# Kernel optimization log

Hardware: AMD Instinct MI355X
Metric: run time of the kernel (lower is better)

The kernel has to match this reference:

```python
import jax, jax.numpy as jnp
import numpy as np

N = 50000      # nodes
E = 1600000    # edges (before self loops)
F = 128        # input_dim
H = 4          # num_heads
D = 32         # hidden_dim (per head)
B = 16         # graphs in batch
NEG_SLOPE = 0.2  # PyG GATv2Conv default negative_slope


def setup_inputs() -> dict:
    key = jax.random.key(0)
    ks = jax.random.split(key, 8)
    x = jax.random.normal(ks[0], (N, F), dtype=jnp.float32)
    edge_index = jax.random.randint(ks[1], (2, E), 0, N, dtype=jnp.int32)
    batch = jnp.sort(jax.random.randint(ks[2], (N,), 0, B, dtype=jnp.int32))
    s = 0.05
    W_l = jax.random.normal(ks[3], (F, H * D), dtype=jnp.float32) * s
    b_l = jnp.zeros((H * D,), dtype=jnp.float32)
    W_r = jax.random.normal(ks[4], (F, H * D), dtype=jnp.float32) * s
    b_r = jnp.zeros((H * D,), dtype=jnp.float32)
    att = jax.random.normal(ks[5], (H, D), dtype=jnp.float32) * s
    bias = jnp.zeros((H * D,), dtype=jnp.float32)
    return {"x": x, "edge_index": edge_index, "batch": batch,
            "W_l": W_l, "b_l": b_l, "W_r": W_r, "b_r": b_r,
            "att": att, "bias": bias}


def reference(x, edge_index, batch, W_l, b_l, W_r, b_r, att, bias):
    n = x.shape[0]
    # PyG GATv2Conv adds self loops by default
    loops = jnp.arange(n, dtype=edge_index.dtype)
    src = jnp.concatenate([edge_index[0], loops])  # message source j
    dst = jnp.concatenate([edge_index[1], loops])  # message target i

    xl = (x @ W_l + b_l).reshape(n, H, D)  # source transform
    xr = (x @ W_r + b_r).reshape(n, H, D)  # target transform

    # per-edge GATv2 attention logits: a^T LeakyReLU(xl_j + xr_i)
    m = xl[src] + xr[dst]                                   # [E+N, H, D]
    e = jnp.sum(jax.nn.leaky_relu(m, NEG_SLOPE) * att, -1)  # [E+N, H]

    # softmax over incoming edges of each destination node
    e_max = jax.ops.segment_max(e, dst, num_segments=n)
    ex = jnp.exp(e - e_max[dst])
    den = jax.ops.segment_sum(ex, dst, num_segments=n)
    alpha = ex / den[dst]                                   # [E+N, H]

    # weighted scatter-sum aggregation of source features
    out = jax.ops.segment_sum(alpha[..., None] * xl[src], dst, num_segments=n)
    out = out.reshape(n, H * D) + bias                      # concat heads + bias
    out = jax.nn.relu(out)

    # global max pool over nodes of each graph
    pooled = jax.ops.segment_max(out, batch, num_segments=B)
    pooled = jnp.where(jnp.isfinite(pooled), pooled, 0.0)   # guard empty graphs
    return pooled
```

## Files before the change

kernel.cpp:

```cpp
#include <hip/hip_runtime.h>

#define NN 50000
#define NE 1600000
#define FDIM 128
#define CDIM 128
#define NGRAPH 16
#define SLOPE 0.2f
#define CSTRIDE 96
#define BINSH 7
#define NBIN 391
#define EPB 6400
#define NB1 250
#define EPT 25
#define CAP 5120
#define POOL_NODES 64
#define POOL_NB ((NN + POOL_NODES - 1) / POOL_NODES)
#define TNB 782
#define LOG2E 1.4426950408889634f


__device__ __forceinline__ unsigned short f2bf(float f) {
    unsigned u = __float_as_uint(f);
    return (unsigned short)((u + 0x7FFFu + ((u >> 16) & 1u)) >> 16);
}
__device__ __forceinline__ unsigned packbf(float a, float b) {
    return (unsigned)f2bf(a) | ((unsigned)f2bf(b) << 16);
}
__device__ __forceinline__ unsigned short f2h(float f) {
    union { _Float16 h; unsigned short u; } c;
    c.h = (_Float16)f;
    return c.u;
}

typedef __attribute__((ext_vector_type(8))) short short8;
typedef __attribute__((ext_vector_type(4))) float f32x4;
typedef _Float16 h2 __attribute__((ext_vector_type(2)));
union FragU { uint4 u; short8 s; };
union HU    { uint4 u; h2 h[4]; };
union HI    { h2 h; int i; };

__device__ __forceinline__ float qadd_xor1(float d) {
#if __has_builtin(__builtin_amdgcn_update_dpp)
    int x = __builtin_amdgcn_update_dpp(0, __float_as_int(d), 0xB1, 0xF, 0xF, true);
    return d + __int_as_float(x);
#else
    return d + __shfl_xor(d, 1);
#endif
}
__device__ __forceinline__ float qadd_xor2(float d) {
#if __has_builtin(__builtin_amdgcn_update_dpp)
    int x = __builtin_amdgcn_update_dpp(0, __float_as_int(d), 0x4E, 0xF, 0xF, true);
    return d + __int_as_float(x);
#else
    return d + __shfl_xor(d, 2);
#endif
}
__device__ __forceinline__ float exp2fast(float d) {
#if __has_builtin(__builtin_amdgcn_exp2f)
    return __builtin_amdgcn_exp2f(d);
#else
    return __expf(d * 0.6931471805599453f);
#endif
}

__global__ __launch_bounds__(256) void k_init(
    float* __restrict__ out, int* __restrict__ gbin_cnt,
    const float* __restrict__ Wl, const float* __restrict__ Wr,
    uint4* __restrict__ wpack) {
    const int b = blockIdx.x;
    if (b < 16) {
        int C = b * 256 + threadIdx.x;
        const float* W = (C < 2048) ? Wl : Wr;
        int c = C & 2047;
        int ccol = c & 15, cq = (c >> 4) & 3, ckq = (c >> 6) & 3, cnt_ = c >> 8;
        const float* wp = &W[(size_t)(ckq * 32 + cq * 8) * CDIM + cnt_ * 16 + ccol];
        uint4 u;
        u.x = packbf(wp[0],        wp[CDIM]);
        u.y = packbf(wp[2*CDIM],   wp[3*CDIM]);
        u.z = packbf(wp[4*CDIM],   wp[5*CDIM]);
        u.w = packbf(wp[6*CDIM],   wp[7*CDIM]);
        wpack[C] = u;
    } else {
        int i = (b - 16) * 256 + threadIdx.x;
        if (i < NGRAPH * CDIM) out[i] = 0.f;
        if (i < NBIN) gbin_cnt[i] = 0;
    }
}

__global__ __launch_bounds__(256) void k_front(
    const float* __restrict__ x,
    const float* __restrict__ bl, const float* __restrict__ br,
    const int* __restrict__ src, const int* __restrict__ dst,
    int* __restrict__ gbin_cnt, unsigned* __restrict__ gstage,
    unsigned short* __restrict__ xlh, unsigned short* __restrict__ xrh,
    const uint4* __restrict__ wpack) {
    __shared__ __align__(16) char shraw[32768];
    const int tid = threadIdx.x;

    if (blockIdx.x < NB1) {
        int* bcnt = (int*)shraw;
        int* boff = bcnt + NBIN;
        int* gb   = boff + NBIN;
        int* sc   = gb + NBIN;
        unsigned* st = (unsigned*)(sc + 256);
        const int t  = tid;
        const int e0 = blockIdx.x * EPB;

        for (int b = t; b < NBIN; b += 256) bcnt[b] = 0;
        __syncthreads();

        unsigned sd[EPT]; int bn[EPT]; int pl[EPT];
#pragma unroll
        for (int k = 0; k < EPT; k++) {
            int e = e0 + k * 256 + t;
            int s = src[e], d = dst[e];
            bn[k] = d >> BINSH;
            sd[k] = (unsigned)s | ((unsigned)(d & 127) << 16)
                                | ((unsigned)bn[k] << 23);
            pl[k] = atomicAdd(&bcnt[bn[k]], 1);
        }
        __syncthreads();

        int c0 = (2*t     < NBIN) ? bcnt[2*t]     : 0;
        int c1 = (2*t + 1 < NBIN) ? bcnt[2*t + 1] : 0;
        int v  = c0 + c1;
        sc[t] = v; __syncthreads();
        for (int off = 1; off < 256; off <<= 1) {
            int add = (t >= off) ? sc[t - off] : 0;
            __syncthreads();
            sc[t] += add;
            __syncthreads();
        }
        int base = sc[t] - v;
        if (2*t     < NBIN) boff[2*t]     = base;
        if (2*t + 1 < NBIN) boff[2*t + 1] = base + c0;
        __syncthreads();

        for (int b = t; b < NBIN; b += 256) {
            int c = bcnt[b];
            gb[b] = (c > 0) ? atomicAdd(&gbin_cnt[b], c) : 0;
        }
#pragma unroll
        for (int k = 0; k < EPT; k++) st[boff[bn[k]] + pl[k]] = sd[k];
        __syncthreads();

        for (int idx = t; idx < EPB; idx += 256) {
            unsigned w = st[idx];
            int b = w >> 23;
            int p = gb[b] + (idx - boff[b]);
            if (p < CAP) gstage[(size_t)b * CAP + p] = w;
        }
    } else {
        uint4* wfrag = (uint4*)shraw;
        const int bid   = blockIdx.x - NB1;
        const int wv    = tid >> 6;
        const int lane  = tid & 63;
        const int quad  = lane >> 4;
        const int col   = lane & 15;
        const int node0 = bid * 64;
        const int nodeA = node0 + wv * 16 + col;
        const bool aval = nodeA < NN;

        FragU afrag[4];
#pragma unroll
        for (int kq = 0; kq < 4; kq++) {
            float4 lo = make_float4(0.f,0.f,0.f,0.f), hi = lo;
            if (aval) {
                const float* ap = &x[(size_t)nodeA * FDIM + kq * 32 + quad * 8];
                lo = *(const float4*)ap;
                hi = *(const float4*)(ap + 4);
            }
            afrag[kq].u.x = packbf(lo.x, lo.y);
            afrag[kq].u.y = packbf(lo.z, lo.w);
            afrag[kq].u.z = packbf(hi.x, hi.y);
            afrag[kq].u.w = packbf(hi.z, hi.w);
        }

        const int myrow0 = node0 + wv * 16 + quad * 4;

        for (int mat = 0; mat < 2; mat++) {
            const float* bb = mat ? br : bl;
            unsigned short* dsto = mat ? xrh : xlh;
            const uint4* wsrc = wpack + mat * 2048;
            __syncthreads();
#pragma unroll
            for (int i = 0; i < 8; i++)
                wfrag[i * 256 + tid] = wsrc[i * 256 + tid];
            __syncthreads();

#pragma unroll
            for (int nt = 0; nt < 8; nt++) {
                f32x4 acc = {0.f, 0.f, 0.f, 0.f};
#pragma unroll
                for (int kq = 0; kq < 4; kq++) {
                    FragU bfr;
                    bfr.u = wfrag[(nt * 4 + kq) * 64 + lane];
                    acc = __builtin_amdgcn_mfma_f32_16x16x32_bf16(
                              afrag[kq].s, bfr.s, acc, 0, 0, 0);
                }
                int ch = nt * 16 + col;
                float bv = bb[ch];
#pragma unroll
                for (int r = 0; r < 4; r++) {
                    int node = myrow0 + r;
                    if (node < NN)
                        dsto[(size_t)node * CDIM + ch] = f2h(acc[r] + bv);
                }
            }
        }
    }
}

__global__ __launch_bounds__(512) void k_csr(
    const int* __restrict__ gbin_cnt, const unsigned* __restrict__ gstage,
    int* __restrict__ cnt, unsigned short* __restrict__ colp) {
    __shared__ int nfill[128];
    __shared__ unsigned short crow[128 * CSTRIDE];
    const int bin = blockIdx.x;
    const int t   = threadIdx.x;
    const int n0  = bin << BINSH;
    const int nb  = min(128, NN - n0);
    const int m   = min(gbin_cnt[bin], CAP);

    if (t < 128) nfill[t] = 0;
    __syncthreads();

    unsigned w[10];
    bool     ok[10];
#pragma unroll
    for (int k = 0; k < 10; k++) {
        int i = k * 512 + t;
        ok[k] = i < m;
        if (ok[k]) w[k] = gstage[(size_t)bin * CAP + i];
    }
#pragma unroll
    for (int k = 0; k < 10; k++) {
        if (ok[k]) {
            int dl = (w[k] >> 16) & 127;
            int p  = atomicAdd(&nfill[dl], 1);
            if (p < CSTRIDE - 1)
                crow[dl * CSTRIDE + p] = (unsigned short)(w[k] & 0xFFFF);
        }
    }
    __syncthreads();

    if (t < nb) {
        int c = min(nfill[t], CSTRIDE - 1);
        crow[t * CSTRIDE + c] = (unsigned short)(n0 + t);
        cnt[n0 + t] = c + 1;
    }
    __syncthreads();

    unsigned* gout = (unsigned*)colp + (size_t)bin * (128 * CSTRIDE / 2);
    const unsigned* cin = (const unsigned*)crow;
    for (int idx = t; idx < 128 * CSTRIDE / 2; idx += 512) gout[idx] = cin[idx];
}

__device__ __forceinline__ void edge_compute(
    uint4 qu,
    const h2* __restrict__ rx, const h2* __restrict__ ah,
    float& s, h2* __restrict__ acch) {
    HU q; q.u = qu;
    const h2 c02 = {(_Float16)SLOPE, (_Float16)SLOPE};
    float d = 0.f;
#pragma unroll
    for (int k = 0; k < 4; k++) {
        h2 t  = q.h[k] + rx[k];
        h2 lk = __builtin_elementwise_max(t, t * c02);
#if __has_builtin(__builtin_amdgcn_fdot2)
        d = __builtin_amdgcn_fdot2(lk, ah[k], d, false);
#else
        d = fmaf((float)lk.x, (float)ah[k].x, d);
        d = fmaf((float)lk.y, (float)ah[k].y, d);
#endif
    }
    d = qadd_xor1(d);
    d = qadd_xor2(d);
    float w = exp2fast(d);
    s += w;
    _Float16 wh = (_Float16)w;
    h2 w2 = {wh, wh};
#pragma unroll
    for (int k = 0; k < 4; k++)
        acch[k] += w2 * q.h[k];
}

__device__ __forceinline__ void edge_body(
    const char* __restrict__ xlb, unsigned chb, int j,
    const h2* __restrict__ rx, const h2* __restrict__ ah,
    float& s, h2* __restrict__ acch) {
    uint4 qu = *(const uint4*)(xlb + (((unsigned)j << 8) | chb));
    edge_compute(qu, rx, ah, s, acch);
}

__global__ __launch_bounds__(256) void k_aggregate(
    const unsigned short* __restrict__ xlh, const unsigned short* __restrict__ xrh,
    const float* __restrict__ att, const float* __restrict__ bias,
    const int* __restrict__ cnt, const unsigned short* __restrict__ colp,
    float* __restrict__ nodeout) {
    const int wave = blockIdx.x * 4 + (threadIdx.x >> 6);
    const int lane = threadIdx.x & 63;
    const int i     = wave;
    const size_t start = (size_t)i * CSTRIDE;
    const int deg   = cnt[i];
    const int grp   = lane >> 4;
    const int ch0   = (lane & 15) * 8;
    const unsigned chb = (unsigned)(ch0 * 2);
    const char* xlb = (const char*)xlh;

    int cj0 = (int)colp[start + lane];
    int cj1 = 0;
    if (deg > 64) cj1 = (int)colp[start + 64 + lane];

    HU rxu;
    rxu.u = *(const uint4*)&xrh[(size_t)i * CDIM + ch0];
    const float4 aa0 = *(const float4*)&att[ch0];
    const float4 aa1 = *(const float4*)&att[ch0 + 4];
    h2 ah[4];
    ah[0] = h2{(_Float16)(aa0.x*LOG2E), (_Float16)(aa0.y*LOG2E)};
    ah[1] = h2{(_Float16)(aa0.z*LOG2E), (_Float16)(aa0.w*LOG2E)};
    ah[2] = h2{(_Float16)(aa1.x*LOG2E), (_Float16)(aa1.y*LOG2E)};
    ah[3] = h2{(_Float16)(aa1.z*LOG2E), (_Float16)(aa1.w*LOG2E)};

    float s = 0.f;
    h2 acch[4];
#pragma unroll
    for (int k = 0; k < 4; k++) acch[k] = h2{(_Float16)0.f, (_Float16)0.f};

    const int full = deg >> 2;
    const int f0   = full < 16 ? full : 16;

    if (f0 > 0) {
        int ja = __shfl(cj0, grp);
        uint4 qa = *(const uint4*)(xlb + (((unsigned)ja << 8) | chb));
        if (f0 > 1) {
            int jb = __shfl(cj0, 4 + grp);
            uint4 qb = *(const uint4*)(xlb + (((unsigned)jb << 8) | chb));
            for (int t = 0; t + 2 < f0; t++) {
                int jc = __shfl(cj0, (t + 2) * 4 + grp);
                uint4 qc = *(const uint4*)(xlb + (((unsigned)jc << 8) | chb));
                edge_compute(qa, rxu.h, ah, s, acch);
                qa = qb; qb = qc;
            }
            edge_compute(qa, rxu.h, ah, s, acch);
            edge_compute(qb, rxu.h, ah, s, acch);
        } else {
            edge_compute(qa, rxu.h, ah, s, acch);
        }
    }
    for (int t = 16; t < full; t++) {
        int j = __shfl(cj1, t * 4 + grp - 64);
        edge_body(xlb, chb, j, rxu.h, ah, s, acch);
    }
    int e  = full * 4 + grp;
    int jt = (e < 64) ? __shfl(cj0, e) : __shfl(cj1, (e - 64) & 63);
    if (e < deg)
        edge_body(xlb, chb, jt, rxu.h, ah, s, acch);

#pragma unroll
    for (int dist = 16; dist <= 32; dist <<= 1) {
        s += __shfl_xor(s, dist);
#pragma unroll
        for (int k = 0; k < 4; k++) {
            HI a, b;
            a.h = acch[k];
            b.i = __shfl_xor(a.i, dist);
            acch[k] = a.h + b.h;
        }
    }

    if (grp == 0) {
        float inv = 1.f / s;
        float4 o0, o1;
        const float4 b0 = *(const float4*)&bias[ch0];
        const float4 b1 = *(const float4*)&bias[ch0 + 4];
        o0.x = fmaxf(fmaf((float)acch[0].x, inv, b0.x), 0.f);
        o0.y = fmaxf(fmaf((float)acch[0].y, inv, b0.y), 0.f);
        o0.z = fmaxf(fmaf((float)acch[1].x, inv, b0.z), 0.f);
        o0.w = fmaxf(fmaf((float)acch[1].y, inv, b0.w), 0.f);
        o1.x = fmaxf(fmaf((float)acch[2].x, inv, b1.x), 0.f);
        o1.y = fmaxf(fmaf((float)acch[2].y, inv, b1.y), 0.f);
        o1.z = fmaxf(fmaf((float)acch[3].x, inv, b1.z), 0.f);
        o1.w = fmaxf(fmaf((float)acch[3].y, inv, b1.w), 0.f);
        float* op = &nodeout[(size_t)i * CDIM + ch0];
        *(float4*)op       = o0;
        *(float4*)(op + 4) = o1;
    }
}

__global__ __launch_bounds__(256) void k_pool(
    const float* __restrict__ nodeout, const int* __restrict__ batch,
    float* __restrict__ out) {
    const int tid  = threadIdx.x;
    const int c4   = (tid & 31) * 4;
    const int nl   = tid >> 5;
    const int base = blockIdx.x * POOL_NODES;
    float4 mx = make_float4(0.f, 0.f, 0.f, 0.f);
    int cur = -1;
#pragma unroll
    for (int k = 0; k < POOL_NODES / 8; k++) {
        int node = base + k * 8 + nl;
        if (node >= NN) break;
        int g = batch[node];
        if (g != cur) {
            if (cur >= 0) {
                int* op = (int*)&out[cur * CDIM + c4];
                if (mx.x > 0.f) atomicMax(op,     __float_as_int(mx.x));
                if (mx.y > 0.f) atomicMax(op + 1, __float_as_int(mx.y));
                if (mx.z > 0.f) atomicMax(op + 2, __float_as_int(mx.z));
                if (mx.w > 0.f) atomicMax(op + 3, __float_as_int(mx.w));
            }
            cur = g;
            mx = make_float4(0.f, 0.f, 0.f, 0.f);
        }
        float4 v = *(const float4*)&nodeout[(size_t)node * CDIM + c4];
        mx.x = fmaxf(mx.x, v.x);
        mx.y = fmaxf(mx.y, v.y);
        mx.z = fmaxf(mx.z, v.z);
        mx.w = fmaxf(mx.w, v.w);
    }
    if (cur >= 0) {
        int* op = (int*)&out[cur * CDIM + c4];
        if (mx.x > 0.f) atomicMax(op,     __float_as_int(mx.x));
        if (mx.y > 0.f) atomicMax(op + 1, __float_as_int(mx.y));
        if (mx.z > 0.f) atomicMax(op + 2, __float_as_int(mx.z));
        if (mx.w > 0.f) atomicMax(op + 3, __float_as_int(mx.w));
    }
}

extern "C" void kernel_launch(void* const* d_in, const int* in_sizes, int n_in,
                              void* d_out, int out_size, void* d_ws, size_t ws_size,
                              hipStream_t stream) {
    const float* x     = (const float*)d_in[0];
    const int*   ei    = (const int*)d_in[1];
    const int*   batch = (const int*)d_in[2];
    const float* Wl    = (const float*)d_in[3];
    const float* bl    = (const float*)d_in[4];
    const float* Wr    = (const float*)d_in[5];
    const float* br    = (const float*)d_in[6];
    const float* att   = (const float*)d_in[7];
    const float* bias  = (const float*)d_in[8];
    float* out = (float*)d_out;

    char* w = (char*)d_ws;
    float*          nodeout  = (float*)w;          w += (size_t)NN * CDIM * 4;
    unsigned short* xlh      = (unsigned short*)w; w += (size_t)NN * CDIM * 2;
    unsigned short* xrh      = (unsigned short*)w; w += (size_t)NN * CDIM * 2;
    int*            cnt      = (int*)w;            w += (size_t)NN * 4;
    unsigned short* colp     = (unsigned short*)w; w += (size_t)NBIN * 128 * CSTRIDE * 2;
    unsigned*       gstage   = (unsigned*)w;       w += (size_t)NBIN * CAP * 4;
    int*            gbin_cnt = (int*)w;            w += (size_t)NBIN * 4;
    uint4*          wpack    = (uint4*)w;          w += (size_t)4096 * 16;

    const int* src = ei;
    const int* dst = ei + NE;

    k_init<<<26, 256, 0, stream>>>(out, gbin_cnt, Wl, Wr, wpack);
    k_front<<<NB1 + TNB, 256, 0, stream>>>(x, bl, br,
                                           src, dst, gbin_cnt, gstage, xlh, xrh,
                                           wpack);
    k_csr<<<NBIN, 512, 0, stream>>>(gbin_cnt, gstage, cnt, colp);
    k_aggregate<<<NN / 4, 256, 0, stream>>>(xlh, xrh, att, bias,
                                            cnt, colp, nodeout);
    k_pool<<<POOL_NB, 256, 0, stream>>>(nodeout, batch, out);
}
```

Baseline: 226.3 us.

## Store node outputs as fp16, deepen gather prefetch, use nontemporal stores

```diff
diff --git a/kernel.cpp b/kernel.cpp
--- a/kernel.cpp
+++ b/kernel.cpp
@@ -34,10 +34,22 @@
 
 typedef __attribute__((ext_vector_type(8))) short short8;
 typedef __attribute__((ext_vector_type(4))) float f32x4;
+typedef unsigned uintx4 __attribute__((ext_vector_type(4)));
 typedef _Float16 h2 __attribute__((ext_vector_type(2)));
+typedef __fp16 fp16x2 __attribute__((ext_vector_type(2)));
 union FragU { uint4 u; short8 s; };
 union HU    { uint4 u; h2 h[4]; };
 union HI    { h2 h; int i; };
+union HW    { unsigned u; h2 h; };
+union PK    { fp16x2 p; unsigned u; };
+
+__device__ __forceinline__ unsigned pkh(float a, float b) {
+#if __has_builtin(__builtin_amdgcn_cvt_pkrtz)
+    PK c; c.p = __builtin_amdgcn_cvt_pkrtz(a, b); return c.u;
+#else
+    return (unsigned)f2h(a) | ((unsigned)f2h(b) << 16);
+#endif
+}
 
 __device__ __forceinline__ float qadd_xor1(float d) {
 #if __has_builtin(__builtin_amdgcn_update_dpp)
@@ -204,7 +216,9 @@
                 for (int r = 0; r < 4; r++) {
                     int node = myrow0 + r;
                     if (node < NN)
-                        dsto[(size_t)node * CDIM + ch] = f2h(acc[r] + bv);
+                        __builtin_nontemporal_store(
+                            f2h(acc[r] + bv),
+                            &dsto[(size_t)node * CDIM + ch]);
                 }
             }
         }
@@ -297,7 +311,7 @@
     const unsigned short* __restrict__ xlh, const unsigned short* __restrict__ xrh,
     const float* __restrict__ att, const float* __restrict__ bias,
     const int* __restrict__ cnt, const unsigned short* __restrict__ colp,
-    float* __restrict__ nodeout) {
+    unsigned short* __restrict__ nodeout) {
     const int wave = blockIdx.x * 4 + (threadIdx.x >> 6);
     const int lane = threadIdx.x & 63;
     const int i     = wave;
@@ -333,15 +347,23 @@
     if (f0 > 0) {
         int ja = __shfl(cj0, grp);
         uint4 qa = *(const uint4*)(xlb + (((unsigned)ja << 8) | chb));
-        if (f0 > 1) {
+        if (f0 > 2) {
             int jb = __shfl(cj0, 4 + grp);
             uint4 qb = *(const uint4*)(xlb + (((unsigned)jb << 8) | chb));
-            for (int t = 0; t + 2 < f0; t++) {
-                int jc = __shfl(cj0, (t + 2) * 4 + grp);
-                uint4 qc = *(const uint4*)(xlb + (((unsigned)jc << 8) | chb));
+            int jc = __shfl(cj0, 8 + grp);
+            uint4 qc = *(const uint4*)(xlb + (((unsigned)jc << 8) | chb));
+            for (int t = 0; t + 3 < f0; t++) {
+                int jd = __shfl(cj0, (t + 3) * 4 + grp);
+                uint4 qd = *(const uint4*)(xlb + (((unsigned)jd << 8) | chb));
                 edge_compute(qa, rxu.h, ah, s, acch);
-                qa = qb; qb = qc;
+                qa = qb; qb = qc; qc = qd;
             }
+            edge_compute(qa, rxu.h, ah, s, acch);
+            edge_compute(qb, rxu.h, ah, s, acch);
+            edge_compute(qc, rxu.h, ah, s, acch);
+        } else if (f0 == 2) {
+            int jb = __shfl(cj0, 4 + grp);
+            uint4 qb = *(const uint4*)(xlb + (((unsigned)jb << 8) | chb));
             edge_compute(qa, rxu.h, ah, s, acch);
             edge_compute(qb, rxu.h, ah, s, acch);
         } else {
@@ -371,31 +393,31 @@
 
     if (grp == 0) {
         float inv = 1.f / s;
-        float4 o0, o1;
         const float4 b0 = *(const float4*)&bias[ch0];
         const float4 b1 = *(const float4*)&bias[ch0 + 4];
-        o0.x = fmaxf(fmaf((float)acch[0].x, inv, b0.x), 0.f);
-        o0.y = fmaxf(fmaf((float)acch[0].y, inv, b0.y), 0.f);
-        o0.z = fmaxf(fmaf((float)acch[1].x, inv, b0.z), 0.f);
-        o0.w = fmaxf(fmaf((float)acch[1].y, inv, b0.w), 0.f);
-        o1.x = fmaxf(fmaf((float)acch[2].x, inv, b1.x), 0.f);
-        o1.y = fmaxf(fmaf((float)acch[2].y, inv, b1.y), 0.f);
-        o1.z = fmaxf(fmaf((float)acch[3].x, inv, b1.z), 0.f);
-        o1.w = fmaxf(fmaf((float)acch[3].y, inv, b1.w), 0.f);
-        float* op = &nodeout[(size_t)i * CDIM + ch0];
-        *(float4*)op       = o0;
-        *(float4*)(op + 4) = o1;
+        float o0 = fmaxf(fmaf((float)acch[0].x, inv, b0.x), 0.f);
+        float o1 = fmaxf(fmaf((float)acch[0].y, inv, b0.y), 0.f);
+        float o2 = fmaxf(fmaf((float)acch[1].x, inv, b0.z), 0.f);
+        float o3 = fmaxf(fmaf((float)acch[1].y, inv, b0.w), 0.f);
+        float o4 = fmaxf(fmaf((float)acch[2].x, inv, b1.x), 0.f);
+        float o5 = fmaxf(fmaf((float)acch[2].y, inv, b1.y), 0.f);
+        float o6 = fmaxf(fmaf((float)acch[3].x, inv, b1.z), 0.f);
+        float o7 = fmaxf(fmaf((float)acch[3].y, inv, b1.w), 0.f);
+        uintx4 pv = {pkh(o0, o1), pkh(o2, o3), pkh(o4, o5), pkh(o6, o7)};
+        __builtin_nontemporal_store(
+            pv, (uintx4*)(nodeout + (size_t)i * CDIM + ch0));
     }
 }
 
 __global__ __launch_bounds__(256) void k_pool(
-    const float* __restrict__ nodeout, const int* __restrict__ batch,
+    const unsigned short* __restrict__ nodeout, const int* __restrict__ batch,
     float* __restrict__ out) {
     const int tid  = threadIdx.x;
     const int c4   = (tid & 31) * 4;
     const int nl   = tid >> 5;
     const int base = blockIdx.x * POOL_NODES;
-    float4 mx = make_float4(0.f, 0.f, 0.f, 0.f);
+    h2 mxa = h2{(_Float16)0.f, (_Float16)0.f};
+    h2 mxb = h2{(_Float16)0.f, (_Float16)0.f};
     int cur = -1;
 #pragma unroll
     for (int k = 0; k < POOL_NODES / 8; k++) {
@@ -404,27 +426,32 @@
         int g = batch[node];
         if (g != cur) {
             if (cur >= 0) {
+                float fx = (float)mxa.x, fy = (float)mxa.y;
+                float fz = (float)mxb.x, fw = (float)mxb.y;
                 int* op = (int*)&out[cur * CDIM + c4];
-                if (mx.x > 0.f) atomicMax(op,     __float_as_int(mx.x));
-                if (mx.y > 0.f) atomicMax(op + 1, __float_as_int(mx.y));
-                if (mx.z > 0.f) atomicMax(op + 2, __float_as_int(mx.z));
-                if (mx.w > 0.f) atomicMax(op + 3, __float_as_int(mx.w));
+                if (fx > 0.f) atomicMax(op,     __float_as_int(fx));
+                if (fy > 0.f) atomicMax(op + 1, __float_as_int(fy));
+                if (fz > 0.f) atomicMax(op + 2, __float_as_int(fz));
+                if (fw > 0.f) atomicMax(op + 3, __float_as_int(fw));
             }
             cur = g;
-            mx = make_float4(0.f, 0.f, 0.f, 0.f);
-        }
-        float4 v = *(const float4*)&nodeout[(size_t)node * CDIM + c4];
-        mx.x = fmaxf(mx.x, v.x);
-        mx.y = fmaxf(mx.y, v.y);
-        mx.z = fmaxf(mx.z, v.z);
-        mx.w = fmaxf(mx.w, v.w);
+            mxa = h2{(_Float16)0.f, (_Float16)0.f};
+            mxb = h2{(_Float16)0.f, (_Float16)0.f};
+        }
+        uint2 v = *(const uint2*)(nodeout + (size_t)node * CDIM + c4);
+        HW wa; wa.u = v.x;
+        HW wb; wb.u = v.y;
+        mxa = __builtin_elementwise_max(mxa, wa.h);
+        mxb = __builtin_elementwise_max(mxb, wb.h);
     }
     if (cur >= 0) {
+        float fx = (float)mxa.x, fy = (float)mxa.y;
+        float fz = (float)mxb.x, fw = (float)mxb.y;
         int* op = (int*)&out[cur * CDIM + c4];
-        if (mx.x > 0.f) atomicMax(op,     __float_as_int(mx.x));
-        if (mx.y > 0.f) atomicMax(op + 1, __float_as_int(mx.y));
-        if (mx.z > 0.f) atomicMax(op + 2, __float_as_int(mx.z));
-        if (mx.w > 0.f) atomicMax(op + 3, __float_as_int(mx.w));
+        if (fx > 0.f) atomicMax(op,     __float_as_int(fx));
+        if (fy > 0.f) atomicMax(op + 1, __float_as_int(fy));
+        if (fz > 0.f) atomicMax(op + 2, __float_as_int(fz));
+        if (fw > 0.f) atomicMax(op + 3, __float_as_int(fw));
     }
 }
 
@@ -443,7 +470,7 @@
     float* out = (float*)d_out;
 
     char* w = (char*)d_ws;
-    float*          nodeout  = (float*)w;          w += (size_t)NN * CDIM * 4;
+    unsigned short* nodeout  = (unsigned short*)w; w += (size_t)NN * CDIM * 2;
     unsigned short* xlh      = (unsigned short*)w; w += (size_t)NN * CDIM * 2;
     unsigned short* xrh      = (unsigned short*)w; w += (size_t)NN * CDIM * 2;
     int*            cnt      = (int*)w;            w += (size_t)NN * 4;
```

Result: no change. 225.8 us (-0.2%).
